# Kernel optimization log

Measured on AMD Instinct MI355X. Metric: run time of the kernel, lower is better.

## Reference

```python
import jax, jax.numpy as jnp
import numpy as np
import math

D_MODEL = 1024
N_HEADS = 16
DEPTH = D_MODEL // N_HEADS
ROPE_BASE = 10000.0
LS_INIT = 1e-05


def _rope_cos_sin(seq_len, depth, dtype=jnp.float32):
    inv_freq = 1.0 / (ROPE_BASE ** (jnp.arange(0, depth, 2, dtype=jnp.float32) / depth))
    t = jnp.arange(seq_len, dtype=jnp.float32)
    freqs = jnp.einsum('i,j->ij', t, inv_freq)          # [S, depth/2]
    emb = jnp.concatenate([freqs, freqs], axis=-1)       # [S, depth]
    return emb.astype(dtype).cos()[None, None], emb.astype(dtype).sin()[None, None]  # wrong order fixed below


def rope_cos_sin(seq_len, depth):
    inv_freq = 1.0 / (ROPE_BASE ** (jnp.arange(0, depth, 2, dtype=jnp.float32) / depth))
    t = jnp.arange(seq_len, dtype=jnp.float32)
    freqs = jnp.einsum('i,j->ij', t, inv_freq)          # [S, depth/2]
    emb = jnp.concatenate([freqs, freqs], axis=-1)       # [S, depth]
    return jnp.cos(emb)[None, None], jnp.sin(emb)[None, None]  # [1,1,S,depth]


def rotate_half(x):
    x1, x2 = jnp.split(x, 2, axis=-1)
    return jnp.concatenate([-x2, x1], axis=-1)


def setup_inputs() -> dict:
    key = jax.random.key(0)
    ks = jax.random.split(key, 6)
    B, S, D = 2, 2048, D_MODEL
    s = 1.0 / math.sqrt(D)
    return {
        'query': jax.random.normal(ks[0], (B, S, D), dtype=jnp.float32),
        'Wq': jax.random.normal(ks[1], (D, D), dtype=jnp.float32) * s,
        'bq': jnp.zeros((D,), jnp.float32),
        'Wk': jax.random.normal(ks[2], (D, D), dtype=jnp.float32) * s,
        'bk': jnp.zeros((D,), jnp.float32),
        'Wv': jax.random.normal(ks[3], (D, D), dtype=jnp.float32) * s,
        'bv': jnp.zeros((D,), jnp.float32),
        'Wo': jax.random.normal(ks[4], (D, D), dtype=jnp.float32) * s,
        'bo': jnp.zeros((D,), jnp.float32),
        'gamma': jnp.full((D,), LS_INIT, jnp.float32),
    }


def reference(query, Wq, bq, Wk, bk, Wv, bv, Wo, bo, gamma):
    B, S, D = query.shape
    H, dh = N_HEADS, DEPTH

    def split_heads(x):  # [B,S,D] -> [B,H,S,dh]
        return x.reshape(B, S, H, dh).transpose(0, 2, 1, 3)

    # torch Linear: x @ W.T + b, W is [out,in]
    q = split_heads(query @ Wq.T + bq)
    k = split_heads(query @ Wk.T + bk)
    v = split_heads(query @ Wv.T + bv)

    cos, sin = rope_cos_sin(S, dh)  # [1,1,S,dh]
    q = q * cos + rotate_half(q) * sin
    k = k * cos + rotate_half(k) * sin

    logits = jnp.einsum('bhqd,bhkd->bhqk', q, k) / math.sqrt(dh)
    attn = jax.nn.softmax(logits, axis=-1)          # dropout = identity (eval)
    out = jnp.einsum('bhqk,bhkd->bhqd', attn, v)    # [B,H,S,dh]
    out = out.transpose(0, 2, 1, 3).reshape(B, S, D)
    out = out @ Wo.T + bo
    return gamma * out
```

## Files before the change

kernel.cpp:

```cpp
#include <hip/hip_runtime.h>
#include <hip/hip_bf16.h>
#include <math.h>

typedef __bf16 bf16_t;
typedef __bf16 bf16x8 __attribute__((ext_vector_type(8)));
typedef __bf16 bf16x4 __attribute__((ext_vector_type(4)));
typedef short short4v __attribute__((ext_vector_type(4)));
typedef float floatx4 __attribute__((ext_vector_type(4)));

#define SC_QK 0.18033688011112042f

__device__ __forceinline__ float fast_exp2(float x) {
#if __has_builtin(__builtin_amdgcn_exp2f)
  return __builtin_amdgcn_exp2f(x);
#else
  return exp2f(x);
#endif
}

__device__ __forceinline__ void async_load16(const bf16_t* g, bf16_t* l) {
  __builtin_amdgcn_global_load_lds(
      (__attribute__((address_space(1))) void*)(void*)g,
      (__attribute__((address_space(3))) void*)l, 16, 0, 0);
}

__device__ __forceinline__ void wait_and_barrier() {
  asm volatile("" ::: "memory");
  __builtin_amdgcn_s_waitcnt(0x0070);
  __builtin_amdgcn_s_barrier();
  asm volatile("" ::: "memory");
}

__device__ __forceinline__ floatx4 mfma_pv(bf16x4 vfrag, bf16x4 pfrag,
                                           floatx4 acc) {
#if __has_builtin(__builtin_amdgcn_mfma_f32_16x16x16bf16_1k)
  return __builtin_amdgcn_mfma_f32_16x16x16bf16_1k(
      __builtin_bit_cast(short4v, vfrag), __builtin_bit_cast(short4v, pfrag),
      acc, 0, 0, 0);
#else
  const bf16_t z = (bf16_t)0.0f;
  bf16x8 a = {vfrag[0], vfrag[1], vfrag[2], vfrag[3], z, z, z, z};
  bf16x8 b = {pfrag[0], pfrag[1], pfrag[2], pfrag[3], z, z, z, z};
  return __builtin_amdgcn_mfma_f32_16x16x32_bf16(a, b, acc, 0, 0, 0);
#endif
}

__global__ __launch_bounds__(256) void convert_kernel(
    const float* __restrict__ query, const float* __restrict__ Wq,
    const float* __restrict__ Wk, const float* __restrict__ Wv,
    const float* __restrict__ Wo, bf16_t* __restrict__ Xbf,
    bf16_t* __restrict__ Wqkv, bf16_t* __restrict__ Wobf,
    float* __restrict__ tab) {
  if (blockIdx.x >= 8192) {
    int idx = (blockIdx.x - 8192) * 256 + threadIdx.x;
    int s = idx >> 5;
    int p = idx & 31;
    float invf = __expf(-(float)p * 0.28782313662425576f);
    float ang = (float)s * invf;
    float c, sn;
    sincosf(ang, &sn, &c);
    tab[idx] = c;
    tab[65536 + idx] = sn;
    return;
  }
  long base = ((long)blockIdx.x * 256 + threadIdx.x) * 4;
  const float* src;
  bf16_t* dst;
  long off;
  if (base < 4194304L)      { src = query; dst = Xbf;             off = base; }
  else if (base < 5242880L) { src = Wq;    dst = Wqkv;            off = base - 4194304L; }
  else if (base < 6291456L) { src = Wk;    dst = Wqkv + 1048576;  off = base - 5242880L; }
  else if (base < 7340032L) { src = Wv;    dst = Wqkv + 2097152;  off = base - 6291456L; }
  else                      { src = Wo;    dst = Wobf;            off = base - 7340032L; }
  float4 v = *reinterpret_cast<const float4*>(src + off);
  dst[off + 0] = (bf16_t)v.x;
  dst[off + 1] = (bf16_t)v.y;
  dst[off + 2] = (bf16_t)v.z;
  dst[off + 3] = (bf16_t)v.w;
}

__device__ __forceinline__ void gemm_tile_db(const bf16_t* __restrict__ A,
                                             const bf16_t* __restrict__ Bn,
                                             int m0, int n0,
                                             floatx4 acc[4][4]) {
  __shared__ __align__(16) bf16_t As[2][4096];
  __shared__ __align__(16) bf16_t Bs[2][4096];
  const int tid = threadIdx.x;
  const int lane = tid & 63;
  const int wave = tid >> 6;
  const int wm = (wave >> 1) * 64;
  const int wn = (wave & 1) * 64;
  const int lr = lane & 15;
  const int lq = lane >> 4;
  const int srow = lane >> 2;
  const int scol = (lane & 3) * 8;

  auto stage = [&](int kk, int p) {
#pragma unroll
    for (int u = 0; u < 2; u++) {
      int t = wave * 2 + u;
      int row = t * 16 + srow;
      async_load16(A + (size_t)(m0 + row) * 1024 + kk + scol, &As[p][t * 512]);
      async_load16(Bn + (size_t)(n0 + row) * 1024 + kk + scol, &Bs[p][t * 512]);
    }
  };

  stage(0, 0);
  for (int it = 0; it < 32; it++) {
    const int p = it & 1;
    wait_and_barrier();
    if (it < 31) stage((it + 1) * 32, p ^ 1);
    bf16x8 af[4], bfr[4];
#pragma unroll
    for (int i = 0; i < 4; i++)
      af[i] = *reinterpret_cast<const bf16x8*>(&As[p][(wm + i * 16 + lr) * 32 + lq * 8]);
#pragma unroll
    for (int j = 0; j < 4; j++)
      bfr[j] = *reinterpret_cast<const bf16x8*>(&Bs[p][(wn + j * 16 + lr) * 32 + lq * 8]);
#pragma unroll
    for (int i = 0; i < 4; i++)
#pragma unroll
      for (int j = 0; j < 4; j++)
        acc[i][j] = __builtin_amdgcn_mfma_f32_16x16x32_bf16(af[i], bfr[j],
                                                            acc[i][j], 0, 0, 0);
  }
}

__global__ __launch_bounds__(256, 3) void qkv_kernel(
    const bf16_t* __restrict__ Xbf, const bf16_t* __restrict__ Wqkv,
    const float* __restrict__ bq, const float* __restrict__ bk,
    const float* __restrict__ bv, const float* __restrict__ Tab,
    bf16_t* __restrict__ Qbuf, bf16_t* __restrict__ Kbuf,
    bf16_t* __restrict__ Vt) {
  const int m0 = blockIdx.x * 128;
  const int n0 = blockIdx.y * 128;
  const int z = blockIdx.z;
  floatx4 acc[4][4];
  floatx4 zero4 = {0.f, 0.f, 0.f, 0.f};
#pragma unroll
  for (int i = 0; i < 4; i++)
#pragma unroll
    for (int j = 0; j < 4; j++) acc[i][j] = zero4;

  gemm_tile_db(Xbf, Wqkv + (size_t)z * 1048576, m0, n0, acc);

  const int lane = threadIdx.x & 63;
  const int wave = threadIdx.x >> 6;
  const int wm = (wave >> 1) * 64;
  const int wn = (wave & 1) * 64;
  const int lr = lane & 15;
  const int lq = lane >> 4;
  const int h = (n0 + wn) >> 6;

  if (z == 2) {
    const int b = m0 >> 11;
    const int sbase = (m0 & 2047) + wm + lq * 4;
#pragma unroll
    for (int i = 0; i < 4; i++)
#pragma unroll
      for (int j = 0; j < 4; j++) {
        int n = n0 + wn + j * 16 + lr;
        int d = j * 16 + lr;
        float bias = bv[n];
        bf16x4 pk;
#pragma unroll
        for (int r = 0; r < 4; r++) pk[r] = (bf16_t)(acc[i][j][r] + bias);
        *reinterpret_cast<bf16x4*>(
            &Vt[((size_t)(b * 16 + h) * 64 + d) * 2048 + sbase + i * 16]) = pk;
      }
  } else {
    bf16_t* dst = (z == 0) ? Qbuf : Kbuf;
    const float* bias = (z == 0) ? bq : bk;
    const float sc = (z == 0) ? SC_QK : 1.0f;
#pragma unroll
    for (int i = 0; i < 4; i++)
#pragma unroll
      for (int r = 0; r < 4; r++) {
        int m = m0 + wm + i * 16 + lq * 4 + r;
        int b = m >> 11, s = m & 2047;
        size_t rowbase = ((size_t)(b * 16 + h) * 2048 + s) * 64;
#pragma unroll
        for (int jj = 0; jj < 2; jj++) {
          int d1 = jj * 16 + lr;
          int n1 = n0 + wn + d1;
          float x1 = acc[i][jj][r] + bias[n1];
          float x2 = acc[i][jj + 2][r] + bias[n1 + 32];
          float c = Tab[s * 32 + d1];
          float sn = Tab[65536 + s * 32 + d1];
          dst[rowbase + d1]      = (bf16_t)((x1 * c - x2 * sn) * sc);
          dst[rowbase + d1 + 32] = (bf16_t)((x2 * c + x1 * sn) * sc);
        }
      }
  }
}

__global__ __launch_bounds__(256, 2) void attn_kernel(
    const bf16_t* __restrict__ Qbuf, const bf16_t* __restrict__ Kbuf,
    const bf16_t* __restrict__ Vt, bf16_t* __restrict__ Ctx) {
  __shared__ __align__(16) bf16_t Sh[2][16384];
  const int tid = threadIdx.x;
  const int lane = tid & 63;
  const int w = tid >> 6;
  const int lr = lane & 15;
  const int lq = lane >> 4;
  const int q0 = blockIdx.x * 128;
  const int bh = blockIdx.y;
  const size_t hb = (size_t)bh * (2048 * 64);
  const int qw = q0 + w * 32;

  bf16x8 qf[2][2];
#pragma unroll
  for (int g = 0; g < 2; g++) {
    const bf16_t* qp = Qbuf + hb + (size_t)(qw + g * 16 + lr) * 64 + lq * 8;
    qf[g][0] = *reinterpret_cast<const bf16x8*>(qp);
    qf[g][1] = *reinterpret_cast<const bf16x8*>(qp + 32);
  }

  floatx4 o[2][4];
  floatx4 lsum4[2];
  floatx4 zero4 = {0.f, 0.f, 0.f, 0.f};
#pragma unroll
  for (int g = 0; g < 2; g++) {
    lsum4[g] = zero4;
#pragma unroll
    for (int dt = 0; dt < 4; dt++) o[g][dt] = zero4;
  }

  const int ksr = lane >> 3;
  const int ksb = lane & 7;
  const int vsr = lane >> 4;
  const int vsb = lane & 15;

  auto stage = [&](int kt, int p) {
    const int k0 = kt * 128;
    bf16_t* Ks = Sh[p];
    bf16_t* Vs = Sh[p] + 8192;
#pragma unroll
    for (int u = 0; u < 4; u++) {
      int t = w * 4 + u;
      {
        int r = t * 8 + ksr;
        int c = ksb ^ (r & 7);
        async_load16(Kbuf + hb + (size_t)(k0 + r) * 64 + c * 8, Ks + t * 512);
      }
      {
        int d = t * 4 + vsr;
        int c = vsb ^ (d & 15);
        async_load16(Vt + hb + (size_t)d * 2048 + k0 + c * 8, Vs + t * 512);
      }
    }
  };

  stage(0, 0);

  for (int kt = 0; kt < 16; kt++) {
    const int p = kt & 1;
    const bf16_t* Ks = Sh[p];
    const bf16_t* Vs = Sh[p] + 8192;

    wait_and_barrier();
    if (kt < 15) stage(kt + 1, p ^ 1);

    bf16x4 pg[2][8];
#pragma unroll
    for (int nt = 0; nt < 8; nt++) {
      int krow = nt * 16 + lr;
      bf16x8 kf0 = *reinterpret_cast<const bf16x8*>(
          &Ks[krow * 64 + (lq ^ (krow & 7)) * 8]);
      bf16x8 kf1 = *reinterpret_cast<const bf16x8*>(
          &Ks[krow * 64 + ((4 + lq) ^ (krow & 7)) * 8]);
#pragma unroll
      for (int g = 0; g < 2; g++) {
        floatx4 z4 = zero4;
        z4 = __builtin_amdgcn_mfma_f32_16x16x32_bf16(kf0, qf[g][0], z4, 0, 0, 0);
        z4 = __builtin_amdgcn_mfma_f32_16x16x32_bf16(kf1, qf[g][1], z4, 0, 0, 0);
#pragma unroll
        for (int r = 0; r < 4; r++) {
          float pv = fast_exp2(z4[r]);
          lsum4[g][r] += pv;
          pg[g][nt][r] = (bf16_t)pv;
        }
      }
    }

#pragma unroll
    for (int nt = 0; nt < 8; nt++) {
      bf16x4 vf[4];
#pragma unroll
      for (int dt = 0; dt < 4; dt++) {
        int d = dt * 16 + lr;
        int blk = (2 * nt + (lq >> 1)) ^ (d & 15);
        vf[dt] = *reinterpret_cast<const bf16x4*>(
            &Vs[d * 128 + blk * 8 + (lq & 1) * 4]);
      }
#pragma unroll
      for (int g = 0; g < 2; g++)
#pragma unroll
        for (int dt = 0; dt < 4; dt++)
          o[g][dt] = mfma_pv(vf[dt], pg[g][nt], o[g][dt]);
    }
  }

  const int b = bh >> 4;
  const int h = bh & 15;
#pragma unroll
  for (int g = 0; g < 2; g++) {
    float l = (lsum4[g][0] + lsum4[g][1]) + (lsum4[g][2] + lsum4[g][3]);
    l += __shfl_xor(l, 16, 64);
    l += __shfl_xor(l, 32, 64);
    float inv_l = 1.0f / l;
    size_t rowb = ((size_t)(b * 2048 + qw + g * 16 + lr)) * 1024 + h * 64;
#pragma unroll
    for (int dt = 0; dt < 4; dt++) {
      bf16x4 pk;
#pragma unroll
      for (int r = 0; r < 4; r++) pk[r] = (bf16_t)(o[g][dt][r] * inv_l);
      *reinterpret_cast<bf16x4*>(&Ctx[rowb + dt * 16 + lq * 4]) = pk;
    }
  }
}

__global__ __launch_bounds__(256, 3) void oproj_kernel(
    const bf16_t* __restrict__ Ctx, const bf16_t* __restrict__ Wobf,
    const float* __restrict__ bo, const float* __restrict__ gamma,
    float* __restrict__ out) {
  const int m0 = blockIdx.x * 128;
  const int n0 = blockIdx.y * 128;
  floatx4 acc[4][4];
  floatx4 zero4 = {0.f, 0.f, 0.f, 0.f};
#pragma unroll
  for (int i = 0; i < 4; i++)
#pragma unroll
    for (int j = 0; j < 4; j++) acc[i][j] = zero4;

  gemm_tile_db(Ctx, Wobf, m0, n0, acc);

  const int lane = threadIdx.x & 63;
  const int wave = threadIdx.x >> 6;
  const int wm = (wave >> 1) * 64;
  const int wn = (wave & 1) * 64;
  const int lr = lane & 15;
  const int lq = lane >> 4;
#pragma unroll
  for (int i = 0; i < 4; i++)
#pragma unroll
    for (int j = 0; j < 4; j++)
#pragma unroll
      for (int r = 0; r < 4; r++) {
        int m = m0 + wm + i * 16 + lq * 4 + r;
        int n = n0 + wn + j * 16 + lr;
        out[(size_t)m * 1024 + n] = gamma[n] * (acc[i][j][r] + bo[n]);
      }
}

extern "C" void kernel_launch(void* const* d_in, const int* in_sizes, int n_in,
                              void* d_out, int out_size, void* d_ws,
                              size_t ws_size, hipStream_t stream) {
  const float* query = (const float*)d_in[0];
  const float* Wq = (const float*)d_in[1];
  const float* bq = (const float*)d_in[2];
  const float* Wk = (const float*)d_in[3];
  const float* bk = (const float*)d_in[4];
  const float* Wv = (const float*)d_in[5];
  const float* bv = (const float*)d_in[6];
  const float* Wo = (const float*)d_in[7];
  const float* bo = (const float*)d_in[8];
  const float* gamma = (const float*)d_in[9];
  float* out = (float*)d_out;

  char* ws = (char*)d_ws;
  bf16_t* Xbf  = (bf16_t*)(ws);
  bf16_t* Wqkv = (bf16_t*)(ws + (8ull << 20));
  bf16_t* Wobf = (bf16_t*)(ws + (14ull << 20));
  bf16_t* Qbuf = (bf16_t*)(ws + (16ull << 20));
  bf16_t* Kbuf = (bf16_t*)(ws + (24ull << 20));
  bf16_t* Vt   = (bf16_t*)(ws + (32ull << 20));
  bf16_t* Ctx  = (bf16_t*)(ws + (40ull << 20));
  float*  Tab  = (float*)(ws + (40ull << 20));

  convert_kernel<<<dim3(8448), dim3(256), 0, stream>>>(query, Wq, Wk, Wv, Wo,
                                                       Xbf, Wqkv, Wobf, Tab);
  qkv_kernel<<<dim3(32, 8, 3), dim3(256), 0, stream>>>(Xbf, Wqkv, bq, bk, bv,
                                                       Tab, Qbuf, Kbuf, Vt);
  attn_kernel<<<dim3(16, 32), dim3(256), 0, stream>>>(Qbuf, Kbuf, Vt, Ctx);
  oproj_kernel<<<dim3(32, 8), dim3(256), 0, stream>>>(Ctx, Wobf, bo, gamma, out);
}
```

Baseline: 197.1 us.

## Enlarge attention blocks to 256 queries and retile output projection to 64x128

The attention kernel now runs 512 threads (8 waves) per block covering 256 queries. Each K/V tile loaded into shared memory is therefore reused by twice as many query rows, and the staging work per wave is halved. The output projection drops the shared GEMM helper for a dedicated 64x128 tile kernel with its own double-buffered async LDS staging, launching twice as many blocks to fill the GPU better. The larger attention block halves the grid to 256 blocks, which risks lower occupancy or poorer load balance across CUs.

New measurement: 198.0 us. About the same (+0.4%).

```diff
diff --git a/kernel.cpp b/kernel.cpp
--- a/kernel.cpp
+++ b/kernel.cpp
@@ -194,7 +194,7 @@
   }
 }
 
-__global__ __launch_bounds__(256, 2) void attn_kernel(
+__global__ __launch_bounds__(512, 2) void attn_kernel(
     const bf16_t* __restrict__ Qbuf, const bf16_t* __restrict__ Kbuf,
     const bf16_t* __restrict__ Vt, bf16_t* __restrict__ Ctx) {
   __shared__ __align__(16) bf16_t Sh[2][16384];
@@ -203,7 +203,7 @@
   const int w = tid >> 6;
   const int lr = lane & 15;
   const int lq = lane >> 4;
-  const int q0 = blockIdx.x * 128;
+  const int q0 = blockIdx.x * 256;
   const int bh = blockIdx.y;
   const size_t hb = (size_t)bh * (2048 * 64);
   const int qw = q0 + w * 32;
@@ -236,8 +236,8 @@
     bf16_t* Ks = Sh[p];
     bf16_t* Vs = Sh[p] + 8192;
 #pragma unroll
-    for (int u = 0; u < 4; u++) {
-      int t = w * 4 + u;
+    for (int u = 0; u < 2; u++) {
+      int t = w * 2 + u;
       {
         int r = t * 8 + ksr;
         int c = ksb ^ (r & 7);
@@ -320,34 +320,72 @@
   }
 }
 
-__global__ __launch_bounds__(256, 3) void oproj_kernel(
+__global__ __launch_bounds__(256, 2) void oproj_kernel(
     const bf16_t* __restrict__ Ctx, const bf16_t* __restrict__ Wobf,
     const float* __restrict__ bo, const float* __restrict__ gamma,
     float* __restrict__ out) {
-  const int m0 = blockIdx.x * 128;
+  __shared__ __align__(16) bf16_t As[2][2048];
+  __shared__ __align__(16) bf16_t Bs[2][4096];
+  const int m0 = blockIdx.x * 64;
   const int n0 = blockIdx.y * 128;
-  floatx4 acc[4][4];
-  floatx4 zero4 = {0.f, 0.f, 0.f, 0.f};
-#pragma unroll
-  for (int i = 0; i < 4; i++)
-#pragma unroll
-    for (int j = 0; j < 4; j++) acc[i][j] = zero4;
-
-  gemm_tile_db(Ctx, Wobf, m0, n0, acc);
-
-  const int lane = threadIdx.x & 63;
-  const int wave = threadIdx.x >> 6;
-  const int wm = (wave >> 1) * 64;
-  const int wn = (wave & 1) * 64;
+  const int tid = threadIdx.x;
+  const int lane = tid & 63;
+  const int wave = tid >> 6;
+  const int wn = wave * 32;
   const int lr = lane & 15;
   const int lq = lane >> 4;
+  const int srow = lane >> 2;
+  const int scol = (lane & 3) * 8;
+
+  floatx4 acc[4][2];
+  floatx4 zero4 = {0.f, 0.f, 0.f, 0.f};
 #pragma unroll
   for (int i = 0; i < 4; i++)
 #pragma unroll
-    for (int j = 0; j < 4; j++)
+    for (int j = 0; j < 2; j++) acc[i][j] = zero4;
+
+  auto stage = [&](int kk, int p) {
+    {
+      int row = wave * 16 + srow;
+      async_load16(Ctx + (size_t)(m0 + row) * 1024 + kk + scol,
+                   &As[p][wave * 512]);
+    }
+#pragma unroll
+    for (int u = 0; u < 2; u++) {
+      int t = wave * 2 + u;
+      int row = t * 16 + srow;
+      async_load16(Wobf + (size_t)(n0 + row) * 1024 + kk + scol,
+                   &Bs[p][t * 512]);
+    }
+  };
+
+  stage(0, 0);
+  for (int it = 0; it < 32; it++) {
+    const int p = it & 1;
+    wait_and_barrier();
+    if (it < 31) stage((it + 1) * 32, p ^ 1);
+    bf16x8 af[4], bfr[2];
+#pragma unroll
+    for (int i = 0; i < 4; i++)
+      af[i] = *reinterpret_cast<const bf16x8*>(&As[p][(i * 16 + lr) * 32 + lq * 8]);
+#pragma unroll
+    for (int j = 0; j < 2; j++)
+      bfr[j] = *reinterpret_cast<const bf16x8*>(&Bs[p][(wn + j * 16 + lr) * 32 + lq * 8]);
+#pragma unroll
+    for (int i = 0; i < 4; i++)
+#pragma unroll
+      for (int j = 0; j < 2; j++)
+        acc[i][j] = __builtin_amdgcn_mfma_f32_16x16x32_bf16(af[i], bfr[j],
+                                                            acc[i][j], 0, 0, 0);
+  }
+
+#pragma unroll
+  for (int i = 0; i < 4; i++)
+#pragma unroll
+    for (int j = 0; j < 2; j++)
 #pragma unroll
       for (int r = 0; r < 4; r++) {
-        int m = m0 + wm + i * 16 + lq * 4 + r;
+        int m = m0 + i * 16 + lq * 4 + r;
         int n = n0 + wn + j * 16 + lr;
         out[(size_t)m * 1024 + n] = gamma[n] * (acc[i][j][r] + bo[n]);
       }
@@ -382,6 +420,6 @@
                                                        Xbf, Wqkv, Wobf, Tab);
   qkv_kernel<<<dim3(32, 8, 3), dim3(256), 0, stream>>>(Xbf, Wqkv, bq, bk, bv,
                                                        Tab, Qbuf, Kbuf, Vt);
-  attn_kernel<<<dim3(16, 32), dim3(256), 0, stream>>>(Qbuf, Kbuf, Vt, Ctx);
-  oproj_kernel<<<dim3(32, 8), dim3(256), 0, stream>>>(Ctx, Wobf, bo, gamma, out);
-}
+  attn_kernel<<<dim3(8, 32), dim3(512), 0, stream>>>(Qbuf, Kbuf, Vt, Ctx);
+  oproj_kernel<<<dim3(64, 8), dim3(256), 0, stream>>>(Ctx, Wobf, bo, gamma, out);
+}
```
